# Kernel optimization log

Measured on AMD Instinct MI355X. Metric: run time of the kernel, lower is better.

The kernel has to match this reference:

```python
import jax, jax.numpy as jnp
import numpy as np

N = 3072      # nodes
D = 256       # embed_dim
H = 8         # heads
E = 98304     # edges (avg degree 32)
B = 16        # graphs in batch


def setup_inputs() -> dict:
    key = jax.random.key(0)
    ks = jax.random.split(key, 14)
    w = lambda k, sh: jax.random.normal(k, sh, jnp.float32) * 0.02
    return {
        "x": jax.random.normal(ks[0], (N, D), jnp.float32),
        "edge_attr": jax.random.normal(ks[1], (E, 4), jnp.float32),
        "Wq": w(ks[2], (D, D)), "bq": jnp.zeros((D,), jnp.float32),
        "Wk": w(ks[3], (D, D)), "bk": jnp.zeros((D,), jnp.float32),
        "Wv": w(ks[4], (D, D)), "bv": jnp.zeros((D,), jnp.float32),
        "Wo": w(ks[5], (D, D)), "bo": jnp.zeros((D,), jnp.float32),
        "We": w(ks[6], (4, H)), "be": jnp.zeros((H,), jnp.float32),
        "edge_index": jax.random.randint(ks[7], (2, E), 0, N),
        "batch": jnp.sort(jax.random.randint(ks[8], (N,), 0, B)),
    }


def reference(x, edge_attr, Wq, bq, Wk, bk, Wv, bv, Wo, bo, We, be,
              edge_index, batch):
    n, d = x.shape
    h = be.shape[0]
    hd = d // h
    # projections -> [h, n, hd]
    Q = (x @ Wq + bq).reshape(n, h, hd).transpose(1, 0, 2)
    K = (x @ Wk + bk).reshape(n, h, hd).transpose(1, 0, 2)
    V = (x @ Wv + bv).reshape(n, h, hd).transpose(1, 0, 2)
    # dense attention scores [h, n, n]
    scores = jnp.einsum('hnd,hmd->hnm', Q, K) / np.float32(np.sqrt(hd))
    # per-edge bias scatter-add (accumulate over duplicate edges)
    edge_bias = edge_attr @ We + be                     # [E, h]
    scores = scores.at[:, edge_index[0], edge_index[1]].add(edge_bias.T)
    # block-diagonal batch mask
    same_graph = batch[:, None] == batch[None, :]       # [n, n]
    scores = jnp.where(same_graph[None], scores, -jnp.inf)
    attn = jax.nn.softmax(scores, axis=-1)              # dropout: eval mode (identity)
    out = jnp.einsum('hnm,hmd->hnd', attn, V)           # [h, n, hd]
    out = out.transpose(1, 0, 2).reshape(n, d)
    return out @ Wo + bo
```

## Files before the change

### kernel.cpp

```cpp
#include <hip/hip_runtime.h>
#include <hip/hip_bf16.h>
#include <math.h>

#define N_NODES 3072
#define DIM     256
#define NH      8
#define HD      32
#define E_EDGES 98304
#define B_GRAPHS 16
#define MAXC    390
#define PADP    392
#define TR      16
#define SCALE   0.17677669529663689f

typedef __attribute__((ext_vector_type(8))) short bf16x8;
typedef __attribute__((ext_vector_type(4))) float f32x4;

__device__ inline unsigned short f2b(float f) {
    __hip_bfloat16 h = __float2bfloat16(f);
    return *reinterpret_cast<unsigned short*>(&h);
}

__global__ void setup_misc(const int* __restrict__ batch, int* __restrict__ counts,
                           int* __restrict__ gstart) {
    int i = blockIdx.x * blockDim.x + threadIdx.x;
    if (i < 2 * N_NODES) counts[i] = 0;
    if (i < N_NODES) {
        int b  = batch[i];
        int bp = (i == 0) ? -1 : batch[i - 1];
        for (int g = bp + 1; g <= b; ++g) gstart[g] = i;
        if (i == N_NODES - 1)
            for (int g = b + 1; g <= B_GRAPHS; ++g) gstart[g] = N_NODES;
    }
}

__global__ __launch_bounds__(256) void qkv_proj(
    const float* __restrict__ x,
    const float* __restrict__ Wq, const float* __restrict__ bq,
    const float* __restrict__ Wk, const float* __restrict__ bk,
    const float* __restrict__ Wv, const float* __restrict__ bv,
    unsigned short* __restrict__ Qb, unsigned short* __restrict__ Kb,
    unsigned short* __restrict__ Vb)
{
    __shared__ float xs[8][DIM];
    const int row0 = blockIdx.x * 8;
    const int t = threadIdx.x;
    for (int i = t; i < 8 * DIM; i += 256) xs[i >> 8][i & 255] = x[(size_t)row0 * DIM + i];
    __syncthreads();

    float accQ[8] = {0,0,0,0,0,0,0,0};
    float accK[8] = {0,0,0,0,0,0,0,0};
    float accV[8] = {0,0,0,0,0,0,0,0};
    const int j = t;
    #pragma unroll 4
    for (int k = 0; k < DIM; ++k) {
        float wq = Wq[k * DIM + j];
        float wk = Wk[k * DIM + j];
        float wv = Wv[k * DIM + j];
        #pragma unroll
        for (int r = 0; r < 8; ++r) {
            float xv = xs[r][k];
            accQ[r] = fmaf(xv, wq, accQ[r]);
            accK[r] = fmaf(xv, wk, accK[r]);
            accV[r] = fmaf(xv, wv, accV[r]);
        }
    }
    float bqv = bq[j], bkv = bk[j], bvv = bv[j];
    #pragma unroll
    for (int r = 0; r < 8; ++r) {
        size_t o = (size_t)(row0 + r) * DIM + j;
        Qb[o] = f2b(accQ[r] + bqv);
        Kb[o] = f2b(accK[r] + bkv);
        Vb[o] = f2b(accV[r] + bvv);
    }
}

__global__ void edge_count(const int* __restrict__ erow, int* __restrict__ counts) {
    int e = blockIdx.x * blockDim.x + threadIdx.x;
    if (e < E_EDGES) atomicAdd(&counts[erow[e]], 1);
}

__global__ __launch_bounds__(1024) void scan_rows(const int* __restrict__ counts,
                                                  int* __restrict__ rowstart) {
    __shared__ int lds[1024];
    const int t = threadIdx.x;
    int c0 = counts[3 * t], c1 = counts[3 * t + 1], c2 = counts[3 * t + 2];
    int local = c0 + c1 + c2;
    lds[t] = local;
    __syncthreads();
    for (int off = 1; off < 1024; off <<= 1) {
        int v = (t >= off) ? lds[t - off] : 0;
        __syncthreads();
        lds[t] += v;
        __syncthreads();
    }
    int incl = lds[t];
    int base = incl - local;
    rowstart[3 * t]     = base;
    rowstart[3 * t + 1] = base + c0;
    rowstart[3 * t + 2] = base + c0 + c1;
    if (t == 1023) rowstart[N_NODES] = incl;
}

__global__ void edge_fill(const int* __restrict__ erow, const int* __restrict__ ecolin,
                          const float* __restrict__ ea, const float* __restrict__ We,
                          const float* __restrict__ be,
                          const int* __restrict__ rowstart, int* __restrict__ cursor,
                          int* __restrict__ ecol, float* __restrict__ ebias) {
    int e = blockIdx.x * blockDim.x + threadIdx.x;
    if (e >= E_EDGES) return;
    int row = erow[e];
    int pos = rowstart[row] + atomicAdd(&cursor[row], 1);
    ecol[pos] = ecolin[e];
    float a0 = ea[e * 4 + 0], a1 = ea[e * 4 + 1], a2 = ea[e * 4 + 2], a3 = ea[e * 4 + 3];
    #pragma unroll
    for (int h = 0; h < NH; ++h) {
        float b = fmaf(a0, We[0 * NH + h],
                  fmaf(a1, We[1 * NH + h],
                  fmaf(a2, We[2 * NH + h],
                  fmaf(a3, We[3 * NH + h], be[h]))));
        ebias[(size_t)h * E_EDGES + pos] = b;
    }
}

__global__ __launch_bounds__(256) void attn(
    const unsigned short* __restrict__ Qb, const unsigned short* __restrict__ Kb,
    const unsigned short* __restrict__ Vb,
    const int* __restrict__ gstart, const int* __restrict__ rowstart,
    const int* __restrict__ ecol, const float* __restrict__ ebias,
    float* __restrict__ pre)
{
    __shared__ float s[TR][MAXC];
    __shared__ unsigned short pb[TR][PADP];
    __shared__ float rowinv[TR];
    __shared__ int   rs_sh[TR + 1];

    const int g = blockIdx.x, tile = blockIdx.y, h = blockIdx.z;
    const int gs = gstart[g], ge = gstart[g + 1];
    const int row0 = gs + tile * TR;
    if (row0 >= ge) return;
    const int nrows = min(TR, ge - row0);
    const int ncols = ge - gs;
    const int cpad  = (ncols + 31) & ~31;
    const int t = threadIdx.x;
    const int wave = t >> 6, lane = t & 63;
    const int l16 = lane & 15, lq = lane >> 4;

    if (t <= nrows) rs_sh[t] = rowstart[row0 + t];

    {
        int arow = min(row0 + l16, N_NODES - 1);
        const bf16x8 aq = *(const bf16x8*)(Qb + (size_t)arow * DIM + h * HD + (lq << 3));
        const int nchunk16 = (ncols + 15) >> 4;
        for (int j = wave; j < nchunk16; j += 4) {
            const int c0 = j << 4;
            int krow = min(gs + c0 + l16, N_NODES - 1);
            bf16x8 bk = *(const bf16x8*)(Kb + (size_t)krow * DIM + h * HD + (lq << 3));
            f32x4 d = {0.f, 0.f, 0.f, 0.f};
            d = __builtin_amdgcn_mfma_f32_16x16x32_bf16(aq, bk, d, 0, 0, 0);
            const int col = c0 + l16, rbase = lq * 4;
            #pragma unroll
            for (int r = 0; r < 4; ++r) s[rbase + r][col] = d[r] * SCALE;
        }
    }
    __syncthreads();

    {
        int e0 = rs_sh[0], e1 = rs_sh[nrows];
        for (int idx = e0 + t; idx < e1; idx += 256) {
            int lo = 0, hi = nrows;
            while (hi - lo > 1) {
                int mid = (lo + hi) >> 1;
                if (rs_sh[mid] <= idx) lo = mid; else hi = mid;
            }
            int col = ecol[idx] - gs;
            if (col >= 0 && col < ncols)
                atomicAdd(&s[lo][col], ebias[(size_t)h * E_EDGES + idx]);
        }
    }
    __syncthreads();

    {
        const int r = t >> 4, sub = t & 15;
        if (r < nrows) {
            float m = -INFINITY;
            for (int c = sub; c < ncols; c += 16) m = fmaxf(m, s[r][c]);
            m = fmaxf(m, __shfl_xor(m, 1, 16));
            m = fmaxf(m, __shfl_xor(m, 2, 16));
            m = fmaxf(m, __shfl_xor(m, 4, 16));
            m = fmaxf(m, __shfl_xor(m, 8, 16));
            float sum = 0.f;
            for (int c = sub; c < cpad; c += 16) {
                if (c < ncols) {
                    float e = __expf(s[r][c] - m);
                    sum += e;
                    pb[r][c] = f2b(e);
                } else {
                    pb[r][c] = 0;
                }
            }
            sum += __shfl_xor(sum, 1, 16);
            sum += __shfl_xor(sum, 2, 16);
            sum += __shfl_xor(sum, 4, 16);
            sum += __shfl_xor(sum, 8, 16);
            if (sub == 0) rowinv[r] = 1.0f / sum;
        } else {
            for (int c = sub; c < cpad; c += 16) pb[r][c] = 0;
        }
    }
    __syncthreads();

    f32x4 o = {0.f, 0.f, 0.f, 0.f};
    {
        const int half = wave >> 1, par = wave & 1;
        const int kout = l16 + (half << 4);
        const int nchunk32 = cpad >> 5;
        for (int j = par; j < nchunk32; j += 2) {
            const int c0 = j << 5;
            bf16x8 ap = *(const bf16x8*)(&pb[l16][c0 + (lq << 3)]);
            bf16x8 bv;
            const int cb = c0 + (lq << 3);
            #pragma unroll
            for (int jj = 0; jj < 8; ++jj) {
                int vr = min(gs + cb + jj, N_NODES - 1);
                bv[jj] = (short)Vb[(size_t)vr * DIM + h * HD + kout];
            }
            o = __builtin_amdgcn_mfma_f32_16x16x32_bf16(ap, bv, o, 0, 0, 0);
        }
    }
    __syncthreads();
    {
        float* red = &s[0][0];
        const int rbase = lq * 4;
        #pragma unroll
        for (int r = 0; r < 4; ++r)
            red[((wave << 4) + rbase + r) * 17 + l16] = o[r];
    }
    __syncthreads();
    {
        const int row = t >> 4, kl = t & 15;
        if (row < nrows) {
            float* red = &s[0][0];
            float v0 = red[(row) * 17 + kl]        + red[(16 + row) * 17 + kl];
            float v1 = red[(32 + row) * 17 + kl]   + red[(48 + row) * 17 + kl];
            float sc = rowinv[row];
            size_t ob = (size_t)(row0 + row) * DIM + h * HD;
            pre[ob + kl]      = v0 * sc;
            pre[ob + 16 + kl] = v1 * sc;
        }
    }
}

__global__ __launch_bounds__(256) void out_proj(
    const float* __restrict__ pre, const float* __restrict__ Wo,
    const float* __restrict__ bo, float* __restrict__ out)
{
    __shared__ float xs[8][DIM];
    const int row0 = blockIdx.x * 8;
    const int t = threadIdx.x;
    for (int i = t; i < 8 * DIM; i += 256) xs[i >> 8][i & 255] = pre[(size_t)row0 * DIM + i];
    __syncthreads();

    float acc[8] = {0,0,0,0,0,0,0,0};
    #pragma unroll 4
    for (int k = 0; k < DIM; ++k) {
        float w = Wo[k * DIM + t];
        #pragma unroll
        for (int r = 0; r < 8; ++r) acc[r] = fmaf(xs[r][k], w, acc[r]);
    }
    float b = bo[t];
    #pragma unroll
    for (int r = 0; r < 8; ++r) out[(size_t)(row0 + r) * DIM + t] = acc[r] + b;
}

extern "C" void kernel_launch(void* const* d_in, const int* in_sizes, int n_in,
                              void* d_out, int out_size, void* d_ws, size_t ws_size,
                              hipStream_t stream) {
    const float* x   = (const float*)d_in[0];
    const float* ea  = (const float*)d_in[1];
    const float* Wq  = (const float*)d_in[2];  const float* bq = (const float*)d_in[3];
    const float* Wk  = (const float*)d_in[4];  const float* bk = (const float*)d_in[5];
    const float* Wv  = (const float*)d_in[6];  const float* bv = (const float*)d_in[7];
    const float* Wo  = (const float*)d_in[8];  const float* bo = (const float*)d_in[9];
    const float* We  = (const float*)d_in[10]; const float* be = (const float*)d_in[11];
    const int*   eidx  = (const int*)d_in[12];
    const int*   batch = (const int*)d_in[13];
    const int* erow   = eidx;
    const int* ecolin = eidx + E_EDGES;

    unsigned short* Qb = (unsigned short*)d_ws;
    unsigned short* Kb = Qb + (size_t)N_NODES * DIM;
    unsigned short* Vb = Kb + (size_t)N_NODES * DIM;
    float* pre = (float*)(Vb + (size_t)N_NODES * DIM);
    int* counts   = (int*)(pre + (size_t)N_NODES * DIM);
    int* cursor   = counts + N_NODES;
    int* rowstart = cursor + N_NODES;
    int* gstart   = rowstart + (N_NODES + 1);
    int* ecol     = gstart + (B_GRAPHS + 1);
    float* ebias  = (float*)(ecol + E_EDGES);

    setup_misc<<<dim3((2 * N_NODES + 255) / 256), dim3(256), 0, stream>>>(batch, counts, gstart);
    qkv_proj<<<dim3(N_NODES / 8), dim3(256), 0, stream>>>(x, Wq, bq, Wk, bk, Wv, bv, Qb, Kb, Vb);
    edge_count<<<dim3(E_EDGES / 256), dim3(256), 0, stream>>>(erow, counts);
    scan_rows<<<dim3(1), dim3(1024), 0, stream>>>(counts, rowstart);
    edge_fill<<<dim3(E_EDGES / 256), dim3(256), 0, stream>>>(erow, ecolin, ea, We, be,
                                                             rowstart, cursor, ecol, ebias);
    attn<<<dim3(B_GRAPHS, 24, NH), dim3(256), 0, stream>>>(Qb, Kb, Vb, gstart, rowstart,
                                                           ecol, ebias, pre);
    out_proj<<<dim3(N_NODES / 8), dim3(256), 0, stream>>>(pre, Wo, bo, (float*)d_out);
}
```

Before: 185.9 us.

## Move QKV and output projections to split-bf16 MFMA with a fused prep kernel

Replaces the scalar fp32 FMA projection kernels with MFMA bf16 kernels that use a hi/lo split (three MFMAs per tile) to keep close to fp32 accuracy. A new prep kernel splits x into bf16 hi/lo parts, transposes and splits the weights, and absorbs the old setup work. The attention kernel now writes its output as hi/lo bf16 for the output projection. This aims to cut the FP32 ALU cost of the projections, at the price of extra conversion passes and more workspace traffic.

```diff
diff --git a/kernel.cpp b/kernel.cpp
--- a/kernel.cpp
+++ b/kernel.cpp
@@ -15,63 +15,120 @@
 
 typedef __attribute__((ext_vector_type(8))) short bf16x8;
 typedef __attribute__((ext_vector_type(4))) float f32x4;
+typedef __attribute__((ext_vector_type(4))) unsigned short ushort4v;
 
 __device__ inline unsigned short f2b(float f) {
     __hip_bfloat16 h = __float2bfloat16(f);
     return *reinterpret_cast<unsigned short*>(&h);
 }
-
-__global__ void setup_misc(const int* __restrict__ batch, int* __restrict__ counts,
-                           int* __restrict__ gstart) {
-    int i = blockIdx.x * blockDim.x + threadIdx.x;
-    if (i < 2 * N_NODES) counts[i] = 0;
-    if (i < N_NODES) {
-        int b  = batch[i];
-        int bp = (i == 0) ? -1 : batch[i - 1];
-        for (int g = bp + 1; g <= b; ++g) gstart[g] = i;
-        if (i == N_NODES - 1)
-            for (int g = b + 1; g <= B_GRAPHS; ++g) gstart[g] = N_NODES;
-    }
-}
-
-__global__ __launch_bounds__(256) void qkv_proj(
+__device__ inline float b2f(unsigned short u) {
+    __hip_bfloat16 h = *reinterpret_cast<__hip_bfloat16*>(&u);
+    return __bfloat162float(h);
+}
+
+__global__ __launch_bounds__(256) void prep(
     const float* __restrict__ x,
-    const float* __restrict__ Wq, const float* __restrict__ bq,
-    const float* __restrict__ Wk, const float* __restrict__ bk,
-    const float* __restrict__ Wv, const float* __restrict__ bv,
+    const float* __restrict__ Wq, const float* __restrict__ Wk,
+    const float* __restrict__ Wv, const float* __restrict__ Wo,
+    unsigned short* __restrict__ xh, unsigned short* __restrict__ xl,
+    unsigned short* __restrict__ Wth, unsigned short* __restrict__ Wtl,
+    const int* __restrict__ batch, int* __restrict__ counts, int* __restrict__ gstart)
+{
+    const int b = blockIdx.x, t = threadIdx.x;
+    if (b < 768) {
+        const int gid = b * 256 + t;
+        float4 v = ((const float4*)x)[gid];
+        ushort4v h, l;
+        float c[4] = {v.x, v.y, v.z, v.w};
+        #pragma unroll
+        for (int i = 0; i < 4; ++i) {
+            unsigned short hi = f2b(c[i]);
+            h[i] = hi;
+            l[i] = f2b(c[i] - b2f(hi));
+        }
+        ((ushort4v*)xh)[gid] = h;
+        ((ushort4v*)xl)[gid] = l;
+    } else if (b < 1024) {
+        __shared__ float tile[32][33];
+        const int wb = b - 768;
+        const int mat = wb >> 6, tidx = wb & 63;
+        const int tk = (tidx >> 3) * 32, tn = (tidx & 7) * 32;
+        const float* W = (mat == 0) ? Wq : (mat == 1) ? Wk : (mat == 2) ? Wv : Wo;
+        const int kk = t >> 5, nn = t & 31;
+        #pragma unroll
+        for (int p = 0; p < 4; ++p)
+            tile[nn][kk + p * 8] = W[(size_t)(tk + kk + p * 8) * DIM + tn + nn];
+        __syncthreads();
+        const int n = t >> 3, kq = (t & 7) * 4;
+        ushort4v h, l;
+        #pragma unroll
+        for (int i = 0; i < 4; ++i) {
+            float v = tile[n][kq + i];
+            unsigned short hi = f2b(v);
+            h[i] = hi;
+            l[i] = f2b(v - b2f(hi));
+        }
+        size_t o = (size_t)mat * DIM * DIM + (size_t)(tn + n) * DIM + tk + kq;
+        *(ushort4v*)(Wth + o) = h;
+        *(ushort4v*)(Wtl + o) = l;
+    } else {
+        const int i = (b - 1024) * 256 + t;
+        if (i < 2 * N_NODES) counts[i] = 0;
+        if (i < N_NODES) {
+            int bb = batch[i];
+            int bp = (i == 0) ? -1 : batch[i - 1];
+            for (int g = bp + 1; g <= bb; ++g) gstart[g] = i;
+            if (i == N_NODES - 1)
+                for (int g = bb + 1; g <= B_GRAPHS; ++g) gstart[g] = N_NODES;
+        }
+    }
+}
+
+__global__ __launch_bounds__(256) void qkv_mfma(
+    const unsigned short* __restrict__ xh, const unsigned short* __restrict__ xl,
+    const unsigned short* __restrict__ Wth, const unsigned short* __restrict__ Wtl,
+    const float* __restrict__ bq, const float* __restrict__ bk, const float* __restrict__ bv,
     unsigned short* __restrict__ Qb, unsigned short* __restrict__ Kb,
     unsigned short* __restrict__ Vb)
 {
-    __shared__ float xs[8][DIM];
-    const int row0 = blockIdx.x * 8;
-    const int t = threadIdx.x;
-    for (int i = t; i < 8 * DIM; i += 256) xs[i >> 8][i & 255] = x[(size_t)row0 * DIM + i];
-    __syncthreads();
-
-    float accQ[8] = {0,0,0,0,0,0,0,0};
-    float accK[8] = {0,0,0,0,0,0,0,0};
-    float accV[8] = {0,0,0,0,0,0,0,0};
-    const int j = t;
-    #pragma unroll 4
-    for (int k = 0; k < DIM; ++k) {
-        float wq = Wq[k * DIM + j];
-        float wk = Wk[k * DIM + j];
-        float wv = Wv[k * DIM + j];
-        #pragma unroll
-        for (int r = 0; r < 8; ++r) {
-            float xv = xs[r][k];
-            accQ[r] = fmaf(xv, wq, accQ[r]);
-            accK[r] = fmaf(xv, wk, accK[r]);
-            accV[r] = fmaf(xv, wv, accV[r]);
-        }
-    }
-    float bqv = bq[j], bkv = bk[j], bvv = bv[j];
+    const int t = threadIdx.x, w = t >> 6, lane = t & 63;
+    const int l16 = lane & 15, lq = lane >> 4;
+    const int mat = blockIdx.y >> 1;
+    const int rb = blockIdx.x * 32 + (w & 1) * 16;
+    const int nb = (blockIdx.y & 1) * 128 + (w >> 1) * 64;
+    const unsigned short* Wh = Wth + (size_t)mat * DIM * DIM;
+    const unsigned short* Wl = Wtl + (size_t)mat * DIM * DIM;
+
+    f32x4 acc[4] = {{0,0,0,0},{0,0,0,0},{0,0,0,0},{0,0,0,0}};
+    const size_t arow = (size_t)(rb + l16) * DIM + (lq << 3);
+
     #pragma unroll
-    for (int r = 0; r < 8; ++r) {
-        size_t o = (size_t)(row0 + r) * DIM + j;
-        Qb[o] = f2b(accQ[r] + bqv);
-        Kb[o] = f2b(accK[r] + bkv);
-        Vb[o] = f2b(accV[r] + bvv);
+    for (int kc = 0; kc < 8; ++kc) {
+        const int k = kc * 32;
+        bf16x8 ah = *(const bf16x8*)(xh + arow + k);
+        bf16x8 al = *(const bf16x8*)(xl + arow + k);
+        #pragma unroll
+        for (int ct = 0; ct < 4; ++ct) {
+            const size_t bo_ = (size_t)(nb + ct * 16 + l16) * DIM + k + (lq << 3);
+            bf16x8 bh = *(const bf16x8*)(Wh + bo_);
+            bf16x8 bl = *(const bf16x8*)(Wl + bo_);
+            acc[ct] = __builtin_amdgcn_mfma_f32_16x16x32_bf16(ah, bh, acc[ct], 0, 0, 0);
+            acc[ct] = __builtin_amdgcn_mfma_f32_16x16x32_bf16(ah, bl, acc[ct], 0, 0, 0);
+            acc[ct] = __builtin_amdgcn_mfma_f32_16x16x32_bf16(al, bh, acc[ct], 0, 0, 0);
+        }
+    }
+
+    const float* bias = (mat == 0) ? bq : (mat == 1) ? bk : bv;
+    unsigned short* outp = (mat == 0) ? Qb : (mat == 1) ? Kb : Vb;
+    #pragma unroll
+    for (int ct = 0; ct < 4; ++ct) {
+        const int n = nb + ct * 16 + l16;
+        const float bvl = bias[n];
+        #pragma unroll
+        for (int r = 0; r < 4; ++r) {
+            const int row = rb + lq * 4 + r;
+            outp[(size_t)row * DIM + n] = f2b(acc[ct][r] + bvl);
+        }
     }
 }
 
@@ -128,7 +185,7 @@
     const unsigned short* __restrict__ Vb,
     const int* __restrict__ gstart, const int* __restrict__ rowstart,
     const int* __restrict__ ecol, const float* __restrict__ ebias,
-    float* __restrict__ pre)
+    unsigned short* __restrict__ preh, unsigned short* __restrict__ prel)
 {
     __shared__ float s[TR][MAXC];
     __shared__ unsigned short pb[TR][PADP];
@@ -245,32 +302,57 @@
             float v1 = red[(32 + row) * 17 + kl]   + red[(48 + row) * 17 + kl];
             float sc = rowinv[row];
             size_t ob = (size_t)(row0 + row) * DIM + h * HD;
-            pre[ob + kl]      = v0 * sc;
-            pre[ob + 16 + kl] = v1 * sc;
-        }
-    }
-}
-
-__global__ __launch_bounds__(256) void out_proj(
-    const float* __restrict__ pre, const float* __restrict__ Wo,
+            float f0 = v0 * sc, f1 = v1 * sc;
+            unsigned short h0 = f2b(f0), h1 = f2b(f1);
+            preh[ob + kl]      = h0;
+            preh[ob + 16 + kl] = h1;
+            prel[ob + kl]      = f2b(f0 - b2f(h0));
+            prel[ob + 16 + kl] = f2b(f1 - b2f(h1));
+        }
+    }
+}
+
+__global__ __launch_bounds__(256) void out_mfma(
+    const unsigned short* __restrict__ preh, const unsigned short* __restrict__ prel,
+    const unsigned short* __restrict__ Wth, const unsigned short* __restrict__ Wtl,
     const float* __restrict__ bo, float* __restrict__ out)
 {
-    __shared__ float xs[8][DIM];
-    const int row0 = blockIdx.x * 8;
-    const int t = threadIdx.x;
-    for (int i = t; i < 8 * DIM; i += 256) xs[i >> 8][i & 255] = pre[(size_t)row0 * DIM + i];
-    __syncthreads();
-
-    float acc[8] = {0,0,0,0,0,0,0,0};
-    #pragma unroll 4
-    for (int k = 0; k < DIM; ++k) {
-        float w = Wo[k * DIM + t];
-        #pragma unroll
-        for (int r = 0; r < 8; ++r) acc[r] = fmaf(xs[r][k], w, acc[r]);
-    }
-    float b = bo[t];
+    const int t = threadIdx.x, w = t >> 6, lane = t & 63;
+    const int l16 = lane & 15, lq = lane >> 4;
+    const int rb = blockIdx.x * 16;
+    const int nb = blockIdx.y * 128 + w * 32;
+    const unsigned short* Wh = Wth + (size_t)3 * DIM * DIM;
+    const unsigned short* Wl = Wtl + (size_t)3 * DIM * DIM;
+
+    f32x4 acc[2] = {{0,0,0,0},{0,0,0,0}};
+    const size_t arow = (size_t)(rb + l16) * DIM + (lq << 3);
+
     #pragma unroll
-    for (int r = 0; r < 8; ++r) out[(size_t)(row0 + r) * DIM + t] = acc[r] + b;
+    for (int kc = 0; kc < 8; ++kc) {
+        const int k = kc * 32;
+        bf16x8 ah = *(const bf16x8*)(preh + arow + k);
+        bf16x8 al = *(const bf16x8*)(prel + arow + k);
+        #pragma unroll
+        for (int ct = 0; ct < 2; ++ct) {
+            const size_t bo_ = (size_t)(nb + ct * 16 + l16) * DIM + k + (lq << 3);
+            bf16x8 bh = *(const bf16x8*)(Wh + bo_);
+            bf16x8 bl = *(const bf16x8*)(Wl + bo_);
+            acc[ct] = __builtin_amdgcn_mfma_f32_16x16x32_bf16(ah, bh, acc[ct], 0, 0, 0);
+            acc[ct] = __builtin_amdgcn_mfma_f32_16x16x32_bf16(ah, bl, acc[ct], 0, 0, 0);
+            acc[ct] = __builtin_amdgcn_mfma_f32_16x16x32_bf16(al, bh, acc[ct], 0, 0, 0);
+        }
+    }
+
+    #pragma unroll
+    for (int ct = 0; ct < 2; ++ct) {
+        const int n = nb + ct * 16 + l16;
+        const float bvl = bo[n];
+        #pragma unroll
+        for (int r = 0; r < 4; ++r) {
+            const int row = rb + lq * 4 + r;
+            out[(size_t)row * DIM + n] = acc[ct][r] + bvl;
+        }
+    }
 }
 
 extern "C" void kernel_launch(void* const* d_in, const int* in_sizes, int n_in,
@@ -288,24 +370,34 @@
     const int* erow   = eidx;
     const int* ecolin = eidx + E_EDGES;
 
-    unsigned short* Qb = (unsigned short*)d_ws;
-    unsigned short* Kb = Qb + (size_t)N_NODES * DIM;
-    unsigned short* Vb = Kb + (size_t)N_NODES * DIM;
-    float* pre = (float*)(Vb + (size_t)N_NODES * DIM);
-    int* counts   = (int*)(pre + (size_t)N_NODES * DIM);
+    const size_t ND = (size_t)N_NODES * DIM;
+    const size_t WD = (size_t)DIM * DIM;
+
+    unsigned short* Qb   = (unsigned short*)d_ws;
+    unsigned short* Kb   = Qb + ND;
+    unsigned short* Vb   = Kb + ND;
+    unsigned short* preh = Vb + ND;
+    unsigned short* prel = preh + ND;
+    unsigned short* xh   = prel + ND;
+    unsigned short* xl   = xh + ND;
+    unsigned short* Wth  = xl + ND;
+    unsigned short* Wtl  = Wth + 4 * WD;
+    int* counts   = (int*)(Wtl + 4 * WD);
     int* cursor   = counts + N_NODES;
     int* rowstart = cursor + N_NODES;
     int* gstart   = rowstart + (N_NODES + 1);
     int* ecol     = gstart + (B_GRAPHS + 1);
     float* ebias  = (float*)(ecol + E_EDGES);
 
-    setup_misc<<<dim3((2 * N_NODES + 255) / 256), dim3(256), 0, stream>>>(batch, counts, gstart);
-    qkv_proj<<<dim3(N_NODES / 8), dim3(256), 0, stream>>>(x, Wq, bq, Wk, bk, Wv, bv, Qb, Kb, Vb);
+    prep<<<dim3(1048), dim3(256), 0, stream>>>(x, Wq, Wk, Wv, Wo, xh, xl, Wth, Wtl,
+                                               batch, counts, gstart);
+    qkv_mfma<<<dim3(96, 6), dim3(256), 0, stream>>>(xh, xl, Wth, Wtl, bq, bk, bv,
+                                                    Qb, Kb, Vb);
     edge_count<<<dim3(E_EDGES / 256), dim3(256), 0, stream>>>(erow, counts);
     scan_rows<<<dim3(1), dim3(1024), 0, stream>>>(counts, rowstart);
     edge_fill<<<dim3(E_EDGES / 256), dim3(256), 0, stream>>>(erow, ecolin, ea, We, be,
                                                              rowstart, cursor, ecol, ebias);
     attn<<<dim3(B_GRAPHS, 24, NH), dim3(256), 0, stream>>>(Qb, Kb, Vb, gstart, rowstart,
-                                                           ecol, ebias, pre);
-    out_proj<<<dim3(N_NODES / 8), dim3(256), 0, stream>>>(pre, Wo, bo, (float*)d_out);
-}
+                                                           ecol, ebias, preh, prel);
+    out_mfma<<<dim3(192, 2), dim3(256), 0, stream>>>(preh, prel, Wth, Wtl, bo, (float*)d_out);
+}
```

Measured after the change: 175.7 us. -5.5%, faster.
